# Performance work log

Measured on AMD Instinct MI355X. Metric: run time of the kernel, lower is better.

The kernel has to match this reference:

```python
import jax, jax.numpy as jnp
import numpy as np

# Mamba2 config (from AdapterMamba: d_model=1024, n_layer=4, headdim=32; mamba_ssm defaults)
D_MODEL = 1024
N_LAYER = 4
EXPAND = 2
HEADDIM = 32
D_STATE = 128
D_CONV = 4
NGROUPS = 1
D_INNER = EXPAND * D_MODEL            # 2048
NHEADS = D_INNER // HEADDIM           # 64
CONV_DIM = D_INNER + 2 * NGROUPS * D_STATE   # 2304
D_IN_PROJ = 2 * D_INNER + 2 * NGROUPS * D_STATE + NHEADS  # 4416
BATCH, SEQLEN = 4, 2048


def setup_inputs() -> dict:
    key = jax.random.key(0)
    ks = jax.random.split(key, 8)
    x = jax.random.normal(ks[0], (BATCH, SEQLEN, D_MODEL), jnp.float32)
    s_in = 1.0 / np.sqrt(D_MODEL)
    s_out = 1.0 / np.sqrt(D_INNER)
    W_in = jax.random.normal(ks[1], (N_LAYER, D_MODEL, D_IN_PROJ), jnp.float32) * s_in
    conv_w = jax.random.normal(ks[2], (N_LAYER, CONV_DIM, D_CONV), jnp.float32) * 0.5
    conv_b = jnp.zeros((N_LAYER, CONV_DIM), jnp.float32)
    # dt_bias = softplus^{-1}(dt) for dt in [1e-3, 0.1] (mamba dt_init)
    dt = jax.random.uniform(ks[3], (N_LAYER, NHEADS), jnp.float32, 0.001, 0.1)
    dt_bias = jnp.log(jnp.expm1(dt))
    # A in [1, 16] per head (A_init_range)
    A_log = jnp.log(jax.random.uniform(ks[4], (N_LAYER, NHEADS), jnp.float32, 1.0, 16.0))
    D = jnp.ones((N_LAYER, NHEADS), jnp.float32)
    gate_norm_w = jnp.ones((N_LAYER, D_INNER), jnp.float32)
    W_out = jax.random.normal(ks[5], (N_LAYER, D_INNER, D_MODEL), jnp.float32) * s_out
    block_norm_w = jnp.ones((N_LAYER, D_MODEL), jnp.float32)
    final_norm_w = jnp.ones((D_MODEL,), jnp.float32)
    return dict(x=x, W_in=W_in, conv_w=conv_w, conv_b=conv_b, dt_bias=dt_bias,
                A_log=A_log, D=D, gate_norm_w=gate_norm_w, W_out=W_out,
                block_norm_w=block_norm_w, final_norm_w=final_norm_w)


def _rmsnorm(x, w, eps=1e-5):
    return x * jax.lax.rsqrt(jnp.mean(x * x, axis=-1, keepdims=True) + eps) * w


def _mamba2_layer(h, Wi, cw, cb, dtb, Alog, Dh, gw, Wo):
    B, L, _ = h.shape
    zxbcdt = h @ Wi                                        # [B,L,4416]
    z, xBC, dt = jnp.split(zxbcdt, [D_INNER, D_INNER + CONV_DIM], axis=-1)
    # causal depthwise conv1d, width D_CONV, over (x, B, C) channels
    xp = jnp.pad(xBC, ((0, 0), (D_CONV - 1, 0), (0, 0)))
    conv = cb + sum(xp[:, k:k + L, :] * cw[:, k] for k in range(D_CONV))
    xBC = jax.nn.silu(conv)
    xs, Bm, Cm = jnp.split(xBC, [D_INNER, D_INNER + D_STATE], axis=-1)
    xs = xs.reshape(B, L, NHEADS, HEADDIM)                 # [B,L,H,P]
    dt = jax.nn.softplus(dt + dtb)                         # [B,L,H]
    A = -jnp.exp(Alog)                                     # [H]
    dA = jnp.exp(dt * A)                                   # [B,L,H]
    dtx = dt[..., None] * xs                               # [B,L,H,P]

    def step(hs, inp):
        dA_t, dtx_t, B_t, C_t = inp
        # hs: [B,H,P,N]
        hs = hs * dA_t[:, :, None, None] + dtx_t[..., None] * B_t[:, None, None, :]
        y = jnp.einsum('bhpn,bn->bhp', hs, C_t)
        return hs, y

    h0 = jnp.zeros((B, NHEADS, HEADDIM, D_STATE), h.dtype)
    _, ys = jax.lax.scan(step, h0, (dA.swapaxes(0, 1), dtx.swapaxes(0, 1),
                                    Bm.swapaxes(0, 1), Cm.swapaxes(0, 1)))
    y = ys.swapaxes(0, 1) + Dh[None, None, :, None] * xs   # skip term D*x
    y = y.reshape(B, L, D_INNER)
    y = _rmsnorm(y * jax.nn.silu(z), gw)                   # gated RMSNorm (Mamba2)
    return y @ Wo


def reference(x, W_in, conv_w, conv_b, dt_bias, A_log, D, gate_norm_w, W_out,
              block_norm_w, final_norm_w):
    h = x
    for l in range(N_LAYER):
        h = h + _mamba2_layer(_rmsnorm(h, block_norm_w[l]), W_in[l], conv_w[l],
                              conv_b[l], dt_bias[l], A_log[l], D[l],
                              gate_norm_w[l], W_out[l])
    return _rmsnorm(h, final_norm_w)
```

## Files before the change

### kernel.cpp

```cpp
#include <hip/hip_runtime.h>

typedef unsigned short u16;
typedef __bf16 bf16x8 __attribute__((ext_vector_type(8)));
typedef float f32x4 __attribute__((ext_vector_type(4)));
typedef u16 u16x8 __attribute__((ext_vector_type(8)));

#define NLAYER 4
#define DMODEL 1024
#define DINNER 2048
#define NHEADS 64
#define CONVDIM 2304
#define XBCLD 2368
#define DPROJ 4416
#define DPROJP 4608
#define BATCH 4
#define SEQLEN 2048
#define NTOK 8192
#define QC 64
#define NCH (SEQLEN / QC)

__device__ __forceinline__ u16 f2bf(float f) {
  union { float f; unsigned u; } v; v.f = f;
  return (u16)((v.u + 0x7fffu + ((v.u >> 16) & 1u)) >> 16);
}
__device__ __forceinline__ float bf2f(u16 h) {
  union { unsigned u; float f; } v; v.u = (unsigned)h << 16; return v.f;
}

__device__ __forceinline__ float block_sum256(float v) {
  __shared__ float red[4];
  #pragma unroll
  for (int o = 32; o; o >>= 1) v += __shfl_xor(v, o);
  int t = threadIdx.x;
  if ((t & 63) == 0) red[t >> 6] = v;
  __syncthreads();
  return red[0] + red[1] + red[2] + red[3];
}

__device__ __forceinline__ int swz128(int row, int g) { return (row << 7) + (((g ^ (row & 7)) << 3)); }
__device__ __forceinline__ int swz64(int row, int g)  { return (row << 6) + (((g ^ (row & 7)) << 3)); }

#define GLDS16(g, s) __builtin_amdgcn_global_load_lds( \
    (const __attribute__((address_space(1))) void*)(g), \
    (__attribute__((address_space(3))) void*)(s), 16, 0, 0)

template<int MODE>
__global__ __launch_bounds__(256, 2) void gemm2b_k(
    const u16* __restrict__ A, const u16* __restrict__ Bt,
    float* __restrict__ C, u16* __restrict__ zy, u16* __restrict__ xbc,
    float* __restrict__ dtraw, int K, int nkt) {
  __shared__ __align__(16) u16 smem[4 * 8192];

  const int tid = threadIdx.x;
  const int w = tid >> 6, l = tid & 63;
  const int wm = w >> 1, wn = w & 1;
  const int l16 = l & 15, kg = l >> 4;
  const int lr = l >> 3, lc = l & 7;
  const int swg = lc ^ lr;

  const int gx = gridDim.x;
  const int nwg = gx * gridDim.y;
  int bid = blockIdx.y * gx + blockIdx.x;
  bid = (bid & 7) * (nwg >> 3) + (bid >> 3);
  const int m0 = (bid / gx) << 7;
  const int n0 = (bid % gx) << 7;

  f32x4 acc[4][4] = {};

  auto stage = [&](int buf, int kt) {
    const size_t kb = (size_t)(kt << 6) + (swg << 3);
    u16* da = smem + (buf << 13);
    u16* db = smem + ((2 + buf) << 13);
    #pragma unroll
    for (int j = 0; j < 4; ++j) {
      const int r0 = (w << 5) + (j << 3);
      GLDS16(A + (size_t)(m0 + r0 + lr) * K + kb, da + (r0 << 6));
      GLDS16(Bt + (size_t)(n0 + r0 + lr) * K + kb, db + (r0 << 6));
    }
  };
  auto readA = [&](int cur, int mf, int ks) -> bf16x8 {
    const int r = (wm << 6) + (mf << 4) + l16;
    return *(const bf16x8*)&smem[(cur << 13) + (r << 6) + ((((ks << 2) + kg) ^ (r & 7)) << 3)];
  };
  auto readB = [&](int cur, int nf, int ks) -> bf16x8 {
    const int r = (wn << 6) + (nf << 4) + l16;
    return *(const bf16x8*)&smem[((2 + cur) << 13) + (r << 6) + ((((ks << 2) + kg) ^ (r & 7)) << 3)];
  };

  stage(0, 0);
  __syncthreads();

  for (int kt = 0; kt < nkt; ++kt) {
    const int cur = kt & 1;
    if (kt + 1 < nkt) stage(cur ^ 1, kt + 1);
    bf16x8 af[4][2], bq[4][2];
    #pragma unroll
    for (int mf = 0; mf < 4; ++mf)
      #pragma unroll
      for (int ks = 0; ks < 2; ++ks) af[mf][ks] = readA(cur, mf, ks);
    #pragma unroll
    for (int nf = 0; nf < 4; ++nf)
      #pragma unroll
      for (int ks = 0; ks < 2; ++ks) bq[nf][ks] = readB(cur, nf, ks);
    __builtin_amdgcn_s_setprio(1);
    #pragma unroll
    for (int mf = 0; mf < 4; ++mf)
      #pragma unroll
      for (int nf = 0; nf < 4; ++nf)
        #pragma unroll
        for (int ks = 0; ks < 2; ++ks)
          acc[mf][nf] = __builtin_amdgcn_mfma_f32_16x16x32_bf16(
              af[mf][ks], bq[nf][ks], acc[mf][nf], 0, 0, 0);
    __builtin_amdgcn_s_setprio(0);
    __syncthreads();
  }

  if (MODE == 1) {
    const int nt = n0 >> 7;
    if (nt == 35) return;
    if (nt == 34) {
      if (wn == 0) {
        #pragma unroll
        for (int mf = 0; mf < 4; ++mf) {
          const int row = m0 + (wm << 6) + (mf << 4) + (kg << 2);
          #pragma unroll
          for (int nf = 0; nf < 4; ++nf) {
            const int dc = (nf << 4) + l16;
            #pragma unroll
            for (int r = 0; r < 4; ++r)
              dtraw[(size_t)(row + r) * 64 + dc] = acc[mf][nf][r];
          }
        }
      }
      return;
    }
    #pragma unroll
    for (int mf = 0; mf < 4; ++mf)
      #pragma unroll
      for (int nf = 0; nf < 4; ++nf) {
        const int col = (wn << 6) + (nf << 4) + l16;
        #pragma unroll
        for (int r = 0; r < 4; ++r) {
          const int row = (wm << 6) + (mf << 4) + (kg << 2) + r;
          smem[(row << 7) + (((col >> 3) ^ (row & 7)) << 3) + (col & 7)] = f2bf(acc[mf][nf][r]);
        }
      }
    __syncthreads();
    const int g = l & 15;
    #pragma unroll
    for (int j = 0; j < 8; ++j) {
      const int row = (w << 5) + (j << 2) + (l >> 4);
      u16x8 v = *(const u16x8*)&smem[(row << 7) + ((g ^ (row & 7)) << 3)];
      const size_t grow = (size_t)(m0 + row);
      const int gcol = n0 + (g << 3);
      if (nt < 16) *(u16x8*)&zy[grow * DINNER + gcol] = v;
      else         *(u16x8*)&xbc[grow * XBCLD + (gcol - 2048)] = v;
    }
  } else {
    float* smf = (float*)smem;
    #pragma unroll
    for (int mf = 0; mf < 4; ++mf)
      #pragma unroll
      for (int nf = 0; nf < 4; ++nf) {
        const int col = (wn << 6) + (nf << 4) + l16;
        #pragma unroll
        for (int r = 0; r < 4; ++r) {
          const int row = (wm << 6) + (mf << 4) + (kg << 2) + r;
          smf[(row << 7) + ((((col >> 2) ^ (row & 7)) << 2) | (col & 3))] = acc[mf][nf][r];
        }
      }
    __syncthreads();
    const int g = l & 31;
    #pragma unroll
    for (int j = 0; j < 16; ++j) {
      const int row = (w << 5) + (j << 1) + (l >> 5);
      f32x4 v = *(const f32x4*)&smf[(row << 7) + ((g ^ (row & 7)) << 2)];
      float* cp = &C[(size_t)(m0 + row) * DMODEL + n0 + (g << 2)];
      f32x4 o = *(const f32x4*)cp;
      #pragma unroll
      for (int q = 0; q < 4; ++q) o[q] += v[q];
      *(f32x4*)cp = o;
    }
  }
}

__global__ __launch_bounds__(256) void transpose_cvt_k(
    const float* __restrict__ in, u16* __restrict__ out, int R, int Cin, int Cpad) {
  __shared__ float t[64][65];
  const int c0 = blockIdx.x << 6, r0 = blockIdx.y << 6;
  const int tx = threadIdx.x & 63, ty = threadIdx.x >> 6;
  #pragma unroll
  for (int i = 0; i < 16; ++i) {
    int r = ty + (i << 2);
    int cc = c0 + tx;
    t[r][tx] = (cc < Cin) ? in[(size_t)(r0 + r) * Cin + cc] : 0.f;
  }
  __syncthreads();
  #pragma unroll
  for (int i = 0; i < 16; ++i) {
    int c = ty + (i << 2);
    out[(size_t)(c0 + c) * R + r0 + tx] = f2bf(t[tx][c]);
  }
}

__global__ void copy_k(const float* __restrict__ in, float* __restrict__ out, int n4) {
  int i = blockIdx.x * blockDim.x + threadIdx.x;
  int stride = gridDim.x * blockDim.x;
  for (; i < n4; i += stride)
    *(f32x4*)&out[(size_t)i * 4] = *(const f32x4*)&in[(size_t)i * 4];
}

__global__ __launch_bounds__(256) void rmsnorm_bf16_k(
    const float* __restrict__ in, const float* __restrict__ w, u16* __restrict__ out) {
  const size_t row = blockIdx.x;
  const int t = threadIdx.x;
  f32x4 v = *(const f32x4*)&in[row * DMODEL + t * 4];
  float ss = block_sum256(v[0]*v[0] + v[1]*v[1] + v[2]*v[2] + v[3]*v[3]);
  float sc = rsqrtf(ss * (1.f / DMODEL) + 1e-5f);
  f32x4 wv = *(const f32x4*)&w[t * 4];
  ushort4 o;
  o.x = f2bf(v[0] * sc * wv[0]); o.y = f2bf(v[1] * sc * wv[1]);
  o.z = f2bf(v[2] * sc * wv[2]); o.w = f2bf(v[3] * sc * wv[3]);
  *(ushort4*)&out[row * DMODEL + t * 4] = o;
}

__global__ __launch_bounds__(256) void final_rmsnorm_k(
    const float* __restrict__ in, const float* __restrict__ w, float* __restrict__ out) {
  const size_t row = blockIdx.x;
  const int t = threadIdx.x;
  f32x4 v = *(const f32x4*)&in[row * DMODEL + t * 4];
  float ss = block_sum256(v[0]*v[0] + v[1]*v[1] + v[2]*v[2] + v[3]*v[3]);
  float sc = rsqrtf(ss * (1.f / DMODEL) + 1e-5f);
  f32x4 wv = *(const f32x4*)&w[t * 4];
  f32x4 o;
  #pragma unroll
  for (int j = 0; j < 4; ++j) o[j] = v[j] * sc * wv[j];
  *(f32x4*)&out[row * DMODEL + t * 4] = o;
}

__global__ __launch_bounds__(256) void conv_tr_k(
    const u16* __restrict__ xbc, const float* __restrict__ cw,
    const float* __restrict__ cb, u16* __restrict__ xact, u16* __restrict__ BT) {
  __shared__ __align__(16) u16 xin[67][72];
  __shared__ __align__(16) u16 xtr[64][72];
  const int ch0 = blockIdx.x << 6, tok0 = blockIdx.y << 6;
  const int tid = threadIdx.x;
  const bool bstart = (tok0 & (SEQLEN - 1)) == 0;
  {
    const int rr = tid >> 3, sg = (tid & 7) << 3;
    #pragma unroll
    for (int i = 0; i < 2; ++i) {
      int r = rr + (i << 5);
      if (bstart && r < 3) *(u16x8*)&xin[r][sg] = (u16x8){};
      else *(int4*)&xin[r][sg] = *(const int4*)&xbc[(size_t)(tok0 - 3 + r) * XBCLD + ch0 + sg];
    }
    if (tid < 24) {
      int r = 64 + (tid >> 3), s2 = (tid & 7) << 3;
      *(int4*)&xin[r][s2] = *(const int4*)&xbc[(size_t)(tok0 - 3 + r) * XBCLD + ch0 + s2];
    }
  }
  __syncthreads();
  const int c2 = tid & 31, th = tid >> 5;
  const int c = c2 << 1, tb = th << 3;
  float wv[2][4], bias[2];
  #pragma unroll
  for (int cc = 0; cc < 2; ++cc) {
    bias[cc] = cb[ch0 + c + cc];
    #pragma unroll
    for (int k = 0; k < 4; ++k) wv[cc][k] = cw[(ch0 + c + cc) * 4 + k];
  }
  float m3[2], m2[2], m1[2];
  #pragma unroll
  for (int cc = 0; cc < 2; ++cc) {
    m3[cc] = bf2f(xin[tb][c + cc]);
    m2[cc] = bf2f(xin[tb + 1][c + cc]);
    m1[cc] = bf2f(xin[tb + 2][c + cc]);
  }
  u16 ov[8][2];
  #pragma unroll
  for (int j = 0; j < 8; ++j) {
    #pragma unroll
    for (int cc = 0; cc < 2; ++cc) {
      float xc = bf2f(xin[tb + 3 + j][c + cc]);
      float a = bias[cc] + wv[cc][0]*m3[cc] + wv[cc][1]*m2[cc] + wv[cc][2]*m1[cc] + wv[cc][3]*xc;
      ov[j][cc] = f2bf(a / (1.f + expf(-a)));
      m3[cc] = m2[cc]; m2[cc] = m1[cc]; m1[cc] = xc;
    }
    unsigned pk = (unsigned)ov[j][0] | ((unsigned)ov[j][1] << 16);
    *(unsigned*)&xact[(size_t)(tok0 + tb + j) * CONVDIM + ch0 + c] = pk;
  }
  if (ch0 == 2048 || ch0 == 2112) {
    #pragma unroll
    for (int cc = 0; cc < 2; ++cc) {
      u16x8 v;
      #pragma unroll
      for (int j = 0; j < 8; ++j) v[j] = ov[j][cc];
      *(u16x8*)&xtr[c + cc][tb] = v;
    }
    __syncthreads();
    #pragma unroll
    for (int p = 0; p < 2; ++p) {
      int slot = tid + (p << 8);
      int cc2 = slot >> 3, tseg = slot & 7;
      u16x8 v = *(const u16x8*)&xtr[cc2][tseg << 3];
      *(u16x8*)&BT[(size_t)(ch0 - 2048 + cc2) * NTOK + tok0 + (tseg << 3)] = v;
    }
  }
}

__global__ __launch_bounds__(256, 2) void ssd_local_k(
    const u16* __restrict__ xact, const u16* __restrict__ BT,
    const float* __restrict__ dtraw, const float* __restrict__ dt_bias,
    const float* __restrict__ A_log, const float* __restrict__ Dv,
    u16* __restrict__ ybuf, u16* __restrict__ Sg,
    float* __restrict__ etg, float* __restrict__ decayg) {
  __shared__ __align__(16) u16 Bs[64 * 128];
  __shared__ __align__(16) u16 U[128 * 64];
  __shared__ __align__(16) u16 Xt[32 * 64];
  __shared__ __align__(16) u16 Pl[64 * 64];
  __shared__ float cums[64], dts[64], fac[64];

  const int h = blockIdx.x, ch = blockIdx.y, b = blockIdx.z;
  const int tid = threadIdx.x, w = tid >> 6, l = tid & 63;
  const int l16 = l & 15, kg = l >> 4;
  const size_t tokb = (size_t)b * SEQLEN + (ch << 6);
  const size_t schunk = ((size_t)(b * 64 + h) << 5) + ch;

  const int srow = tid >> 2, sseg = tid & 3;
  int4 creg[4], breg[4], btreg[4];
  #pragma unroll
  for (int i = 0; i < 4; ++i) {
    creg[i] = *(const int4*)&xact[(tokb + srow) * CONVDIM + 2176 + (sseg << 5) + (i << 3)];
    breg[i] = *(const int4*)&xact[(tokb + srow) * CONVDIM + 2048 + (sseg << 5) + (i << 3)];
  }
  const int xtt = tid >> 2, xps = tid & 3;
  int4 xreg = *(const int4*)&xact[(tokb + xtt) * CONVDIM + (h << 5) + (xps << 3)];
  #pragma unroll
  for (int i = 0; i < 4; ++i)
    btreg[i] = *(const int4*)&BT[(size_t)(tid >> 1) * NTOK + tokb + ((((tid & 1) << 2) + i) << 3)];

  #pragma unroll
  for (int i = 0; i < 4; ++i) {
    *(int4*)&U[swz128(srow, (sseg << 2) + i)]  = creg[i];
    *(int4*)&Bs[swz128(srow, (sseg << 2) + i)] = breg[i];
  }
  {
    u16x8 xv = *(const u16x8*)&xreg;
    #pragma unroll
    for (int j = 0; j < 8; ++j) {
      const int pp = (xps << 3) + j;
      Xt[(pp << 6) + ((((xtt >> 3) ^ (pp & 7)) << 3) | (xtt & 7))] = xv[j];
    }
  }

  if (w == 0) {
    float raw = dtraw[(tokb + l) * 64 + h] + dt_bias[h];
    float dtv = raw > 20.f ? raw : log1pf(__expf(raw));
    float cv = -dtv * __expf(A_log[h]);
    #pragma unroll
    for (int d = 1; d < 64; d <<= 1) {
      float o = __shfl_up(cv, d);
      if (l >= d) cv += o;
    }
    float a63 = __shfl(cv, 63);
    cums[l] = cv; dts[l] = dtv; fac[l] = dtv * __expf(a63 - cv);
    etg[(schunk << 6) + l] = __expf(cv);
    if (l == 0) decayg[schunk] = __expf(a63);
  }
  const float Dh = Dv[h];
  __syncthreads();

  f32x4 gacc[4] = {};
  #pragma unroll
  for (int ks = 0; ks < 4; ++ks) {
    bf16x8 ac = *(const bf16x8*)&U[swz128((w << 4) + l16, (ks << 2) + kg)];
    #pragma unroll
    for (int j = 0; j < 4; ++j)
      if (j <= w) {
        bf16x8 bb = *(const bf16x8*)&Bs[swz128((j << 4) + l16, (ks << 2) + kg)];
        gacc[j] = __builtin_amdgcn_mfma_f32_16x16x32_bf16(ac, bb, gacc[j], 0, 0, 0);
      }
  }
  float c_t[4];
  #pragma unroll
  for (int r = 0; r < 4; ++r) c_t[r] = cums[(w << 4) + (kg << 2) + r];
  #pragma unroll
  for (int j = 0; j < 4; ++j) {
    const int s = (j << 4) + l16;
    const float c_s = cums[s], d_s = dts[s];
    #pragma unroll
    for (int r = 0; r < 4; ++r) {
      const int t = (w << 4) + (kg << 2) + r;
      float v = (s <= t) ? gacc[j][r] * __expf(c_t[r] - c_s) * d_s : 0.f;
      Pl[(t << 6) + ((((s >> 3) ^ (t & 7)) << 3) | (s & 7))] = f2bf(v);
    }
  }

  f32x4 y1[2] = {};
  const int nks = (w >> 1) + 1;
  for (int ks = 0; ks < nks; ++ks) {
    bf16x8 ap = *(const bf16x8*)&Pl[swz64((w << 4) + l16, (ks << 2) + kg)];
    #pragma unroll
    for (int pj = 0; pj < 2; ++pj) {
      bf16x8 bx = *(const bf16x8*)&Xt[swz64((pj << 4) + l16, (ks << 2) + kg)];
      y1[pj] = __builtin_amdgcn_mfma_f32_16x16x32_bf16(ap, bx, y1[pj], 0, 0, 0);
    }
  }
  #pragma unroll
  for (int r = 0; r < 4; ++r) {
    const int t = (w << 4) + (kg << 2) + r;
    #pragma unroll
    for (int pj = 0; pj < 2; ++pj) {
      const int p = (pj << 4) + l16;
      float xv = bf2f(Xt[(p << 6) + ((((t >> 3) ^ (p & 7)) << 3) | (t & 7))]);
      ybuf[(tokb + t) * DINNER + (h << 5) + p] = f2bf(y1[pj][r] + Dh * xv);
    }
  }

  __syncthreads();
  #pragma unroll
  for (int i = 0; i < 4; ++i)
    *(int4*)&U[swz64(tid >> 1, ((tid & 1) << 2) + i)] = btreg[i];
  __syncthreads();

  f32x4 sacc[2][2] = {};
  #pragma unroll
  for (int ks = 0; ks < 2; ++ks) {
    float f8[8];
    #pragma unroll
    for (int j = 0; j < 8; ++j) f8[j] = fac[(ks << 5) + (kg << 3) + j];
    #pragma unroll
    for (int pt = 0; pt < 2; ++pt) {
      bf16x8 xr = *(const bf16x8*)&Xt[swz64((pt << 4) + l16, (ks << 2) + kg)];
      bf16x8 xs;
      #pragma unroll
      for (int j = 0; j < 8; ++j) xs[j] = (__bf16)((float)xr[j] * f8[j]);
      #pragma unroll
      for (int nt = 0; nt < 2; ++nt) {
        bf16x8 bb = *(const bf16x8*)&U[swz64(((w << 1) + nt) * 16 + l16, (ks << 2) + kg)];
        sacc[pt][nt] = __builtin_amdgcn_mfma_f32_16x16x32_bf16(xs, bb, sacc[pt][nt], 0, 0, 0);
      }
    }
  }
  u16* sp = Sg + (schunk << 12);
  #pragma unroll
  for (int pt = 0; pt < 2; ++pt)
    #pragma unroll
    for (int nt = 0; nt < 2; ++nt)
      #pragma unroll
      for (int r = 0; r < 4; ++r) {
        const int pr = (pt << 4) + (kg << 2) + r;
        const int n = (w << 5) + (nt << 4) + l16;
        sp[(pr << 7) + n] = f2bf(sacc[pt][nt][r]);
      }
}

__global__ __launch_bounds__(256) void state_scan_k(
    u16* __restrict__ SH, const float* __restrict__ decayg) {
  const int bid = blockIdx.x;
  const size_t base = ((size_t)bid << 17) + ((size_t)threadIdx.x << 4);
  float acc[16] = {};
  u16x8 s0 = *(const u16x8*)&SH[base];
  u16x8 s1 = *(const u16x8*)&SH[base + 8];
  for (int ch = 0; ch < 32; ++ch) {
    const float d = decayg[(bid << 5) + ch];
    u16x8 n0 = {}, n1 = {};
    if (ch + 1 < 32) {
      n0 = *(const u16x8*)&SH[base + ((size_t)(ch + 1) << 12)];
      n1 = *(const u16x8*)&SH[base + ((size_t)(ch + 1) << 12) + 8];
    }
    u16x8 h0, h1;
    #pragma unroll
    for (int j = 0; j < 8; ++j) { h0[j] = f2bf(acc[j]); h1[j] = f2bf(acc[8 + j]); }
    *(u16x8*)&SH[base + ((size_t)ch << 12)] = h0;
    *(u16x8*)&SH[base + ((size_t)ch << 12) + 8] = h1;
    #pragma unroll
    for (int j = 0; j < 8; ++j) {
      acc[j]     = d * acc[j]     + bf2f(s0[j]);
      acc[8 + j] = d * acc[8 + j] + bf2f(s1[j]);
    }
    s0 = n0; s1 = n1;
  }
}

__global__ __launch_bounds__(256) void ssd_cross_k(
    const u16* __restrict__ xact, const u16* __restrict__ Hg,
    const float* __restrict__ etg, u16* __restrict__ ybuf) {
  __shared__ __align__(16) u16 Cs[64 * 128];
  __shared__ __align__(16) u16 Hb[32 * 128];
  __shared__ float etl[64];
  const int h = blockIdx.x, ch = blockIdx.y + 1, b = blockIdx.z;
  const int tid = threadIdx.x, w = tid >> 6, l = tid & 63;
  const int l16 = l & 15, kg = l >> 4;
  const size_t tokb = (size_t)b * SEQLEN + (ch << 6);
  const size_t schunk = ((size_t)(b * 64 + h) << 5) + ch;

  const int srow = tid >> 2, sseg = tid & 3;
  #pragma unroll
  for (int i = 0; i < 4; ++i) {
    int4 v = *(const int4*)&xact[(tokb + srow) * CONVDIM + 2176 + (sseg << 5) + (i << 3)];
    *(int4*)&Cs[swz128(srow, (sseg << 2) + i)] = v;
  }
  const int hp = tid >> 3, hseg = tid & 7;
  #pragma unroll
  for (int i = 0; i < 2; ++i) {
    int4 v = *(const int4*)&Hg[(schunk << 12) + (hp << 7) + (((hseg << 1) + i) << 3)];
    *(int4*)&Hb[swz128(hp, (hseg << 1) + i)] = v;
  }
  if (tid < 64) etl[tid] = etg[(schunk << 6) + tid];
  __syncthreads();

  f32x4 y2[2] = {};
  #pragma unroll
  for (int ks = 0; ks < 4; ++ks) {
    bf16x8 ac = *(const bf16x8*)&Cs[swz128((w << 4) + l16, (ks << 2) + kg)];
    #pragma unroll
    for (int pj = 0; pj < 2; ++pj) {
      bf16x8 bh = *(const bf16x8*)&Hb[swz128((pj << 4) + l16, (ks << 2) + kg)];
      y2[pj] = __builtin_amdgcn_mfma_f32_16x16x32_bf16(ac, bh, y2[pj], 0, 0, 0);
    }
  }
  #pragma unroll
  for (int r = 0; r < 4; ++r) {
    const int t = (w << 4) + (kg << 2) + r;
    const float et = etl[t];
    #pragma unroll
    for (int pj = 0; pj < 2; ++pj) {
      const int p = (pj << 4) + l16;
      const size_t a = (tokb + t) * DINNER + (h << 5) + p;
      ybuf[a] = f2bf(bf2f(ybuf[a]) + et * y2[pj][r]);
    }
  }
}

__global__ __launch_bounds__(256) void gate_rmsnorm_k(
    const u16* __restrict__ y, u16* __restrict__ zy, const float* __restrict__ gw) {
  const size_t row = blockIdx.x;
  const int t = threadIdx.x;
  bf16x8 yv = *(const bf16x8*)&y[row * DINNER + t * 8];
  bf16x8 zv = *(const bf16x8*)&zy[row * DINNER + t * 8];
  float val[8]; float ss = 0.f;
  #pragma unroll
  for (int j = 0; j < 8; ++j) {
    float z = (float)zv[j];
    float v = (float)yv[j] * (z / (1.f + expf(-z)));
    val[j] = v; ss += v * v;
  }
  ss = block_sum256(ss);
  float sc = rsqrtf(ss * (1.f / DINNER) + 1e-5f);
  ushort4 o0, o1;
  o0.x = f2bf(val[0]*sc*gw[t*8+0]); o0.y = f2bf(val[1]*sc*gw[t*8+1]);
  o0.z = f2bf(val[2]*sc*gw[t*8+2]); o0.w = f2bf(val[3]*sc*gw[t*8+3]);
  o1.x = f2bf(val[4]*sc*gw[t*8+4]); o1.y = f2bf(val[5]*sc*gw[t*8+5]);
  o1.z = f2bf(val[6]*sc*gw[t*8+6]); o1.w = f2bf(val[7]*sc*gw[t*8+7]);
  *(ushort4*)&zy[row * DINNER + t * 8] = o0;
  *(ushort4*)&zy[row * DINNER + t * 8 + 4] = o1;
}

extern "C" void kernel_launch(void* const* d_in, const int* in_sizes, int n_in,
                              void* d_out, int out_size, void* d_ws, size_t ws_size,
                              hipStream_t stream) {
  const float* x       = (const float*)d_in[0];
  const float* W_in    = (const float*)d_in[1];
  const float* conv_w  = (const float*)d_in[2];
  const float* conv_b  = (const float*)d_in[3];
  const float* dt_bias = (const float*)d_in[4];
  const float* A_log   = (const float*)d_in[5];
  const float* Dv      = (const float*)d_in[6];
  const float* gate_w  = (const float*)d_in[7];
  const float* W_out   = (const float*)d_in[8];
  const float* block_w = (const float*)d_in[9];
  const float* final_w = (const float*)d_in[10];
  float* out = (float*)d_out;

  char* p = (char*)d_ws;
  auto alloc = [&](size_t bytes) { char* r = p; p += (bytes + 255) & ~(size_t)255; return r; };
  float* hbuf  = (float*)alloc((size_t)NTOK * DMODEL * 4);
  u16*   slabA = (u16*)  alloc((size_t)NTOK * DINNER * 2);
  u16*   slabB = (u16*)  alloc((size_t)NTOK * DINNER * 2);
  u16*   slabC = (u16*)  alloc((size_t)NTOK * CONVDIM * 2);
  u16*   xbc   = (u16*)  alloc((size_t)NTOK * XBCLD * 2);
  float* dtraw = (float*)alloc((size_t)NTOK * NHEADS * 4);
  u16*   BT    = (u16*)  alloc((size_t)128 * NTOK * 2);
  if ((size_t)(p - (char*)d_ws) > ws_size) return;

  u16*   Sg     = (u16*)  alloc((size_t)BATCH * NHEADS * NCH * 4096 * 2);
  float* etg    = (float*)alloc((size_t)BATCH * NHEADS * NCH * 64 * 4);
  float* decayg = (float*)alloc((size_t)BATCH * NHEADS * NCH * 4);
  const bool par = ((size_t)(p - (char*)d_ws) <= ws_size);

  u16* hn   = slabA;
  u16* ybuf = slabA;
  u16* wt   = slabC;
  u16* xact = slabC;

  copy_k<<<2048, 256, 0, stream>>>(x, hbuf, NTOK * DMODEL / 4);

  for (int l = 0; l < NLAYER; ++l) {
    rmsnorm_bf16_k<<<NTOK, 256, 0, stream>>>(hbuf, block_w + l * DMODEL, hn);
    transpose_cvt_k<<<dim3(DPROJP/64, DMODEL/64), 256, 0, stream>>>(
        W_in + (size_t)l * DMODEL * DPROJ, wt, DMODEL, DPROJ, DPROJP);
    gemm2b_k<1><<<dim3(DPROJP/128, NTOK/128), 256, 0, stream>>>(
        hn, wt, nullptr, slabB, xbc, dtraw, DMODEL, DMODEL / 64);
    conv_tr_k<<<dim3(CONVDIM/64, NTOK/64), 256, 0, stream>>>(
        xbc, conv_w + (size_t)l * CONVDIM * 4, conv_b + (size_t)l * CONVDIM, xact, BT);
    if (par) {
      ssd_local_k<<<dim3(NHEADS, NCH, BATCH), 256, 0, stream>>>(
          xact, BT, dtraw, dt_bias + l * NHEADS, A_log + l * NHEADS,
          Dv + l * NHEADS, ybuf, Sg, etg, decayg);
      state_scan_k<<<BATCH * NHEADS, 256, 0, stream>>>(Sg, decayg);
      ssd_cross_k<<<dim3(NHEADS, NCH - 1, BATCH), 256, 0, stream>>>(
          xact, Sg, etg, ybuf);
    }
    gate_rmsnorm_k<<<NTOK, 256, 0, stream>>>(ybuf, slabB, gate_w + (size_t)l * DINNER);
    transpose_cvt_k<<<dim3(DMODEL/64, DINNER/64), 256, 0, stream>>>(
        W_out + (size_t)l * DINNER * DMODEL, wt, DINNER, DMODEL, DMODEL);
    gemm2b_k<0><<<dim3(DMODEL/128, NTOK/128), 256, 0, stream>>>(
        slabB, wt, hbuf, nullptr, nullptr, nullptr, DINNER, DINNER / 64);
  }
  final_rmsnorm_k<<<NTOK, 256, 0, stream>>>(hbuf, final_w, out);
}
```

Before: 1.455 ms.

## Process eight heads per block in SSD kernels to reuse shared B/C tiles

The local and cross chunk SSD kernels now each handle eight heads per block instead of one. The C·B^T Gram matrix, the B and C tiles and the transposed B are loaded and computed once per block, then reused across all eight heads. Only the per-head x slice, dt cumsum and state differ. The cross kernel prefetches the next head's state into registers while it computes the current one. This removes redundant global loads and duplicate MFMA work, but cuts the grid size 8x and raises shared memory use (Xa is 32KB), which may lower occupancy and parallelism.

Measured after the change: 1.334 ms. 1.09x faster.

```diff
diff --git a/kernel.cpp b/kernel.cpp
--- a/kernel.cpp
+++ b/kernel.cpp
@@ -18,6 +18,7 @@
 #define NTOK 8192
 #define QC 64
 #define NCH (SEQLEN / QC)
+#define MH 8
 
 __device__ __forceinline__ u16 f2bf(float f) {
   union { float f; unsigned u; } v; v.f = f;
@@ -316,25 +317,27 @@
     float* __restrict__ etg, float* __restrict__ decayg) {
   __shared__ __align__(16) u16 Bs[64 * 128];
   __shared__ __align__(16) u16 U[128 * 64];
-  __shared__ __align__(16) u16 Xt[32 * 64];
+  __shared__ __align__(16) u16 Xa[256 * 64];
   __shared__ __align__(16) u16 Pl[64 * 64];
-  __shared__ float cums[64], dts[64], fac[64];
-
-  const int h = blockIdx.x, ch = blockIdx.y, b = blockIdx.z;
+  __shared__ float cums8[MH][64], dts8[MH][64], fac8[MH][64];
+
+  const int h0 = blockIdx.x << 3, ch = blockIdx.y, b = blockIdx.z;
   const int tid = threadIdx.x, w = tid >> 6, l = tid & 63;
   const int l16 = l & 15, kg = l >> 4;
   const size_t tokb = (size_t)b * SEQLEN + (ch << 6);
-  const size_t schunk = ((size_t)(b * 64 + h) << 5) + ch;
+  const size_t schunk0 = ((size_t)(b * 64 + h0) << 5) + ch;
 
   const int srow = tid >> 2, sseg = tid & 3;
-  int4 creg[4], breg[4], btreg[4];
+  int4 creg[4], breg[4], btreg[4], xreg[MH];
   #pragma unroll
   for (int i = 0; i < 4; ++i) {
     creg[i] = *(const int4*)&xact[(tokb + srow) * CONVDIM + 2176 + (sseg << 5) + (i << 3)];
     breg[i] = *(const int4*)&xact[(tokb + srow) * CONVDIM + 2048 + (sseg << 5) + (i << 3)];
   }
   const int xtt = tid >> 2, xps = tid & 3;
-  int4 xreg = *(const int4*)&xact[(tokb + xtt) * CONVDIM + (h << 5) + (xps << 3)];
+  #pragma unroll
+  for (int hh = 0; hh < MH; ++hh)
+    xreg[hh] = *(const int4*)&xact[(tokb + xtt) * CONVDIM + ((h0 + hh) << 5) + (xps << 3)];
   #pragma unroll
   for (int i = 0; i < 4; ++i)
     btreg[i] = *(const int4*)&BT[(size_t)(tid >> 1) * NTOK + tokb + ((((tid & 1) << 2) + i) << 3)];
@@ -344,30 +347,33 @@
     *(int4*)&U[swz128(srow, (sseg << 2) + i)]  = creg[i];
     *(int4*)&Bs[swz128(srow, (sseg << 2) + i)] = breg[i];
   }
-  {
-    u16x8 xv = *(const u16x8*)&xreg;
+  #pragma unroll
+  for (int hh = 0; hh < MH; ++hh) {
+    u16x8 xv = *(const u16x8*)&xreg[hh];
     #pragma unroll
     for (int j = 0; j < 8; ++j) {
-      const int pp = (xps << 3) + j;
-      Xt[(pp << 6) + ((((xtt >> 3) ^ (pp & 7)) << 3) | (xtt & 7))] = xv[j];
-    }
-  }
-
-  if (w == 0) {
-    float raw = dtraw[(tokb + l) * 64 + h] + dt_bias[h];
+      const int pp = (hh << 5) + (xps << 3) + j;
+      Xa[(pp << 6) + ((((xtt >> 3) ^ (pp & 7)) << 3) | (xtt & 7))] = xv[j];
+    }
+  }
+
+  #pragma unroll
+  for (int q = 0; q < 2; ++q) {
+    const int hh = (w << 1) + q, hg = h0 + hh;
+    const size_t sch = schunk0 + ((size_t)hh << 5);
+    float raw = dtraw[(tokb + l) * 64 + hg] + dt_bias[hg];
     float dtv = raw > 20.f ? raw : log1pf(__expf(raw));
-    float cv = -dtv * __expf(A_log[h]);
+    float cv = -dtv * __expf(A_log[hg]);
     #pragma unroll
     for (int d = 1; d < 64; d <<= 1) {
       float o = __shfl_up(cv, d);
       if (l >= d) cv += o;
     }
     float a63 = __shfl(cv, 63);
-    cums[l] = cv; dts[l] = dtv; fac[l] = dtv * __expf(a63 - cv);
-    etg[(schunk << 6) + l] = __expf(cv);
-    if (l == 0) decayg[schunk] = __expf(a63);
-  }
-  const float Dh = Dv[h];
+    cums8[hh][l] = cv; dts8[hh][l] = dtv; fac8[hh][l] = dtv * __expf(a63 - cv);
+    etg[(sch << 6) + l] = __expf(cv);
+    if (l == 0) decayg[sch] = __expf(a63);
+  }
   __syncthreads();
 
   f32x4 gacc[4] = {};
@@ -381,78 +387,84 @@
         gacc[j] = __builtin_amdgcn_mfma_f32_16x16x32_bf16(ac, bb, gacc[j], 0, 0, 0);
       }
   }
-  float c_t[4];
-  #pragma unroll
-  for (int r = 0; r < 4; ++r) c_t[r] = cums[(w << 4) + (kg << 2) + r];
-  #pragma unroll
-  for (int j = 0; j < 4; ++j) {
-    const int s = (j << 4) + l16;
-    const float c_s = cums[s], d_s = dts[s];
+  __syncthreads();
+  #pragma unroll
+  for (int i = 0; i < 4; ++i)
+    *(int4*)&U[swz64(tid >> 1, ((tid & 1) << 2) + i)] = btreg[i];
+  __syncthreads();
+
+  for (int hh = 0; hh < MH; ++hh) {
+    const float Dh = Dv[h0 + hh];
+    const size_t sch = schunk0 + ((size_t)hh << 5);
+
+    float c_t[4];
+    #pragma unroll
+    for (int r = 0; r < 4; ++r) c_t[r] = cums8[hh][(w << 4) + (kg << 2) + r];
+    #pragma unroll
+    for (int j = 0; j < 4; ++j) {
+      const int s = (j << 4) + l16;
+      const float c_s = cums8[hh][s], d_s = dts8[hh][s];
+      #pragma unroll
+      for (int r = 0; r < 4; ++r) {
+        const int t = (w << 4) + (kg << 2) + r;
+        float v = (s <= t) ? gacc[j][r] * __expf(c_t[r] - c_s) * d_s : 0.f;
+        Pl[(t << 6) + ((((s >> 3) ^ (t & 7)) << 3) | (s & 7))] = f2bf(v);
+      }
+    }
+
+    f32x4 y1[2] = {};
+    const int nks = (w >> 1) + 1;
+    for (int ks = 0; ks < nks; ++ks) {
+      bf16x8 ap = *(const bf16x8*)&Pl[swz64((w << 4) + l16, (ks << 2) + kg)];
+      #pragma unroll
+      for (int pj = 0; pj < 2; ++pj) {
+        bf16x8 bx = *(const bf16x8*)&Xa[swz64((hh << 5) + (pj << 4) + l16, (ks << 2) + kg)];
+        y1[pj] = __builtin_amdgcn_mfma_f32_16x16x32_bf16(ap, bx, y1[pj], 0, 0, 0);
+      }
+    }
     #pragma unroll
     for (int r = 0; r < 4; ++r) {
       const int t = (w << 4) + (kg << 2) + r;
-      float v = (s <= t) ? gacc[j][r] * __expf(c_t[r] - c_s) * d_s : 0.f;
-      Pl[(t << 6) + ((((s >> 3) ^ (t & 7)) << 3) | (s & 7))] = f2bf(v);
-    }
-  }
-
-  f32x4 y1[2] = {};
-  const int nks = (w >> 1) + 1;
-  for (int ks = 0; ks < nks; ++ks) {
-    bf16x8 ap = *(const bf16x8*)&Pl[swz64((w << 4) + l16, (ks << 2) + kg)];
-    #pragma unroll
-    for (int pj = 0; pj < 2; ++pj) {
-      bf16x8 bx = *(const bf16x8*)&Xt[swz64((pj << 4) + l16, (ks << 2) + kg)];
-      y1[pj] = __builtin_amdgcn_mfma_f32_16x16x32_bf16(ap, bx, y1[pj], 0, 0, 0);
-    }
-  }
-  #pragma unroll
-  for (int r = 0; r < 4; ++r) {
-    const int t = (w << 4) + (kg << 2) + r;
-    #pragma unroll
-    for (int pj = 0; pj < 2; ++pj) {
-      const int p = (pj << 4) + l16;
-      float xv = bf2f(Xt[(p << 6) + ((((t >> 3) ^ (p & 7)) << 3) | (t & 7))]);
-      ybuf[(tokb + t) * DINNER + (h << 5) + p] = f2bf(y1[pj][r] + Dh * xv);
-    }
-  }
-
-  __syncthreads();
-  #pragma unroll
-  for (int i = 0; i < 4; ++i)
-    *(int4*)&U[swz64(tid >> 1, ((tid & 1) << 2) + i)] = btreg[i];
-  __syncthreads();
-
-  f32x4 sacc[2][2] = {};
-  #pragma unroll
-  for (int ks = 0; ks < 2; ++ks) {
-    float f8[8];
-    #pragma unroll
-    for (int j = 0; j < 8; ++j) f8[j] = fac[(ks << 5) + (kg << 3) + j];
-    #pragma unroll
-    for (int pt = 0; pt < 2; ++pt) {
-      bf16x8 xr = *(const bf16x8*)&Xt[swz64((pt << 4) + l16, (ks << 2) + kg)];
-      bf16x8 xs;
-      #pragma unroll
-      for (int j = 0; j < 8; ++j) xs[j] = (__bf16)((float)xr[j] * f8[j]);
-      #pragma unroll
-      for (int nt = 0; nt < 2; ++nt) {
-        bf16x8 bb = *(const bf16x8*)&U[swz64(((w << 1) + nt) * 16 + l16, (ks << 2) + kg)];
-        sacc[pt][nt] = __builtin_amdgcn_mfma_f32_16x16x32_bf16(xs, bb, sacc[pt][nt], 0, 0, 0);
-      }
-    }
-  }
-  u16* sp = Sg + (schunk << 12);
-  #pragma unroll
-  for (int pt = 0; pt < 2; ++pt)
-    #pragma unroll
-    for (int nt = 0; nt < 2; ++nt)
-      #pragma unroll
-      for (int r = 0; r < 4; ++r) {
-        const int pr = (pt << 4) + (kg << 2) + r;
-        const int n = (w << 5) + (nt << 4) + l16;
-        sp[(pr << 7) + n] = f2bf(sacc[pt][nt][r]);
-      }
+      #pragma unroll
+      for (int pj = 0; pj < 2; ++pj) {
+        const int p = (pj << 4) + l16;
+        const int grow = (hh << 5) + p;
+        float xv = bf2f(Xa[(grow << 6) + ((((t >> 3) ^ (grow & 7)) << 3) | (t & 7))]);
+        ybuf[(tokb + t) * DINNER + ((h0 + hh) << 5) + p] = f2bf(y1[pj][r] + Dh * xv);
+      }
+    }
+
+    f32x4 sacc[2][2] = {};
+    #pragma unroll
+    for (int ks = 0; ks < 2; ++ks) {
+      float f8[8];
+      #pragma unroll
+      for (int j = 0; j < 8; ++j) f8[j] = fac8[hh][(ks << 5) + (kg << 3) + j];
+      #pragma unroll
+      for (int pt = 0; pt < 2; ++pt) {
+        bf16x8 xr = *(const bf16x8*)&Xa[swz64((hh << 5) + (pt << 4) + l16, (ks << 2) + kg)];
+        bf16x8 xs;
+        #pragma unroll
+        for (int j = 0; j < 8; ++j) xs[j] = (__bf16)((float)xr[j] * f8[j]);
+        #pragma unroll
+        for (int nt = 0; nt < 2; ++nt) {
+          bf16x8 bb = *(const bf16x8*)&U[swz64(((w << 1) + nt) * 16 + l16, (ks << 2) + kg)];
+          sacc[pt][nt] = __builtin_amdgcn_mfma_f32_16x16x32_bf16(xs, bb, sacc[pt][nt], 0, 0, 0);
+        }
+      }
+    }
+    u16* sp = Sg + (sch << 12);
+    #pragma unroll
+    for (int pt = 0; pt < 2; ++pt)
+      #pragma unroll
+      for (int nt = 0; nt < 2; ++nt)
+        #pragma unroll
+        for (int r = 0; r < 4; ++r) {
+          const int pr = (pt << 4) + (kg << 2) + r;
+          const int n = (w << 5) + (nt << 4) + l16;
+          sp[(pr << 7) + n] = f2bf(sacc[pt][nt][r]);
+        }
+  }
 }
 
 __global__ __launch_bounds__(256) void state_scan_k(
@@ -483,17 +495,17 @@
   }
 }
 
-__global__ __launch_bounds__(256) void ssd_cross_k(
+__global__ __launch_bounds__(256, 2) void ssd_cross_k(
     const u16* __restrict__ xact, const u16* __restrict__ Hg,
     const float* __restrict__ etg, u16* __restrict__ ybuf) {
   __shared__ __align__(16) u16 Cs[64 * 128];
   __shared__ __align__(16) u16 Hb[32 * 128];
   __shared__ float etl[64];
-  const int h = blockIdx.x, ch = blockIdx.y + 1, b = blockIdx.z;
+  const int h0 = blockIdx.x << 3, ch = blockIdx.y + 1, b = blockIdx.z;
   const int tid = threadIdx.x, w = tid >> 6, l = tid & 63;
   const int l16 = l & 15, kg = l >> 4;
   const size_t tokb = (size_t)b * SEQLEN + (ch << 6);
-  const size_t schunk = ((size_t)(b * 64 + h) << 5) + ch;
+  const size_t schunk0 = ((size_t)(b * 64 + h0) << 5) + ch;
 
   const int srow = tid >> 2, sseg = tid & 3;
   #pragma unroll
@@ -502,33 +514,54 @@
     *(int4*)&Cs[swz128(srow, (sseg << 2) + i)] = v;
   }
   const int hp = tid >> 3, hseg = tid & 7;
-  #pragma unroll
-  for (int i = 0; i < 2; ++i) {
-    int4 v = *(const int4*)&Hg[(schunk << 12) + (hp << 7) + (((hseg << 1) + i) << 3)];
-    *(int4*)&Hb[swz128(hp, (hseg << 1) + i)] = v;
-  }
-  if (tid < 64) etl[tid] = etg[(schunk << 6) + tid];
-  __syncthreads();
-
-  f32x4 y2[2] = {};
-  #pragma unroll
-  for (int ks = 0; ks < 4; ++ks) {
-    bf16x8 ac = *(const bf16x8*)&Cs[swz128((w << 4) + l16, (ks << 2) + kg)];
-    #pragma unroll
-    for (int pj = 0; pj < 2; ++pj) {
-      bf16x8 bh = *(const bf16x8*)&Hb[swz128((pj << 4) + l16, (ks << 2) + kg)];
-      y2[pj] = __builtin_amdgcn_mfma_f32_16x16x32_bf16(ac, bh, y2[pj], 0, 0, 0);
-    }
-  }
-  #pragma unroll
-  for (int r = 0; r < 4; ++r) {
-    const int t = (w << 4) + (kg << 2) + r;
-    const float et = etl[t];
-    #pragma unroll
-    for (int pj = 0; pj < 2; ++pj) {
-      const int p = (pj << 4) + l16;
-      const size_t a = (tokb + t) * DINNER + (h << 5) + p;
-      ybuf[a] = f2bf(bf2f(ybuf[a]) + et * y2[pj][r]);
+  int4 hreg[2];
+  float ereg = 0.f;
+  #pragma unroll
+  for (int i = 0; i < 2; ++i)
+    hreg[i] = *(const int4*)&Hg[(schunk0 << 12) + (hp << 7) + (((hseg << 1) + i) << 3)];
+  if (tid < 64) ereg = etg[(schunk0 << 6) + tid];
+  #pragma unroll
+  for (int i = 0; i < 2; ++i) *(int4*)&Hb[swz128(hp, (hseg << 1) + i)] = hreg[i];
+  if (tid < 64) etl[tid] = ereg;
+  __syncthreads();
+
+  for (int hh = 0; hh < MH; ++hh) {
+    if (hh + 1 < MH) {
+      const size_t schn = schunk0 + ((size_t)(hh + 1) << 5);
+      #pragma unroll
+      for (int i = 0; i < 2; ++i)
+        hreg[i] = *(const int4*)&Hg[(schn << 12) + (hp << 7) + (((hseg << 1) + i) << 3)];
+      if (tid < 64) ereg = etg[(schn << 6) + tid];
+    }
+
+    f32x4 y2[2] = {};
+    #pragma unroll
+    for (int ks = 0; ks < 4; ++ks) {
+      bf16x8 ac = *(const bf16x8*)&Cs[swz128((w << 4) + l16, (ks << 2) + kg)];
+      #pragma unroll
+      for (int pj = 0; pj < 2; ++pj) {
+        bf16x8 bh = *(const bf16x8*)&Hb[swz128((pj << 4) + l16, (ks << 2) + kg)];
+        y2[pj] = __builtin_amdgcn_mfma_f32_16x16x32_bf16(ac, bh, y2[pj], 0, 0, 0);
+      }
+    }
+    #pragma unroll
+    for (int r = 0; r < 4; ++r) {
+      const int t = (w << 4) + (kg << 2) + r;
+      const float et = etl[t];
+      #pragma unroll
+      for (int pj = 0; pj < 2; ++pj) {
+        const int p = (pj << 4) + l16;
+        const size_t a = (tokb + t) * DINNER + ((h0 + hh) << 5) + p;
+        ybuf[a] = f2bf(bf2f(ybuf[a]) + et * y2[pj][r]);
+      }
+    }
+
+    if (hh + 1 < MH) {
+      __syncthreads();
+      #pragma unroll
+      for (int i = 0; i < 2; ++i) *(int4*)&Hb[swz128(hp, (hseg << 1) + i)] = hreg[i];
+      if (tid < 64) etl[tid] = ereg;
+      __syncthreads();
     }
   }
 }
@@ -605,11 +638,11 @@
     conv_tr_k<<<dim3(CONVDIM/64, NTOK/64), 256, 0, stream>>>(
         xbc, conv_w + (size_t)l * CONVDIM * 4, conv_b + (size_t)l * CONVDIM, xact, BT);
     if (par) {
-      ssd_local_k<<<dim3(NHEADS, NCH, BATCH), 256, 0, stream>>>(
+      ssd_local_k<<<dim3(NHEADS/MH, NCH, BATCH), 256, 0, stream>>>(
           xact, BT, dtraw, dt_bias + l * NHEADS, A_log + l * NHEADS,
           Dv + l * NHEADS, ybuf, Sg, etg, decayg);
       state_scan_k<<<BATCH * NHEADS, 256, 0, stream>>>(Sg, decayg);
-      ssd_cross_k<<<dim3(NHEADS, NCH - 1, BATCH), 256, 0, stream>>>(
+      ssd_cross_k<<<dim3(NHEADS/MH, NCH - 1, BATCH), 256, 0, stream>>>(
           xact, Sg, etg, ybuf);
     }
     gate_rmsnorm_k<<<NTOK, 256, 0, stream>>>(ybuf, slabB, gate_w + (size_t)l * DINNER);
```
